# Optimization experiments

Hardware: AMD Instinct MI355X
Metric: run time of the kernel (lower is better)

Reference implementation:

```python
import jax, jax.numpy as jnp
import numpy as np

D_IN = 1024
D_OUT = 1024

def setup_inputs() -> dict:
    key = jax.random.key(0)
    kx, kq, kk, kv = jax.random.split(key, 4)
    X = jax.random.normal(kx, (4, 2048, D_IN), dtype=jnp.float32)
    s = 1.0 / np.sqrt(D_IN)
    Wq = jax.random.uniform(kq, (D_IN, D_OUT), jnp.float32, -s, s)
    Wk = jax.random.uniform(kk, (D_IN, D_OUT), jnp.float32, -s, s)
    Wv = jax.random.uniform(kv, (D_IN, D_OUT), jnp.float32, -s, s)
    return {"X": X, "Wq": Wq, "Wk": Wk, "Wv": Wv}

def reference(X, Wq, Wk, Wv):
    # X: [b, s, d_in]; W*: [d_in, d_out] (torch Linear weight transposed)
    B, S, _ = X.shape
    q = jnp.einsum('bsd,de->bse', X, Wq)
    k = jnp.einsum('bsd,de->bse', X, Wk)
    v = jnp.einsum('bsd,de->bse', X, Wv)
    scores = jnp.einsum('bqe,bke->bqk', q, k)  # [b, s, s]
    causal = jnp.triu(jnp.ones((S, S), dtype=bool), k=1)
    scores = jnp.where(causal, -jnp.inf, scores)
    weights = jax.nn.softmax(scores / jnp.sqrt(jnp.asarray(k.shape[-1], scores.dtype)), axis=-1)
    # dropout p=0.0 (eval) -> identity
    return jnp.einsum('bqk,bke->bqe', weights, v)
```

## Files before the change

### kernel.cpp

```cpp
#include <hip/hip_runtime.h>
#include <cstdint>
#include <cmath>

typedef unsigned short u16;
typedef u16   u16x4  __attribute__((ext_vector_type(4)));
typedef u16   u16x8  __attribute__((ext_vector_type(8)));
typedef __bf16 bf16x8 __attribute__((ext_vector_type(8)));
typedef float f32x4  __attribute__((ext_vector_type(4)));

__device__ __forceinline__ u16 f2bf(float f) {
    uint32_t u = __builtin_bit_cast(uint32_t, f);
    u += 0x7fffu + ((u >> 16) & 1u);
    return (u16)(u >> 16);
}
__device__ __forceinline__ float bf2f(u16 v) {
    uint32_t u = ((uint32_t)v) << 16;
    return __builtin_bit_cast(float, u);
}
__device__ __forceinline__ void gload_lds16(const u16* g, u16* l) {
    __builtin_amdgcn_global_load_lds((const __attribute__((address_space(1))) void*)g,
                                     (__attribute__((address_space(3))) void*)l,
                                     16, 0, 0);
}

__global__ __launch_bounds__(256) void prep_kernel(const float* __restrict__ X,
                                                   const float* __restrict__ Wq,
                                                   const float* __restrict__ Wk,
                                                   const float* __restrict__ Wv,
                                                   u16* __restrict__ Xb,
                                                   u16* __restrict__ Wt) {
    __shared__ u16 tile[64 * 72];
    typedef float f4 __attribute__((ext_vector_type(4)));
    const int bid = blockIdx.x;
    if (bid < 8192) {
        const int idx = bid * 256 + threadIdx.x;
        f4 f = ((const f4*)X)[idx];
        u16x4 o;
        o[0] = f2bf(f[0]); o[1] = f2bf(f[1]); o[2] = f2bf(f[2]); o[3] = f2bf(f[3]);
        ((u16x4*)Xb)[idx] = o;
        return;
    }
    const int id = bid - 8192;
    const int z = id >> 8, rem = id & 255;
    const float* W = (z == 0) ? Wq : (z == 1) ? Wk : Wv;
    u16* out = Wt + ((size_t)z << 20);
    const int nt = (rem & 15) * 64, kt = (rem >> 4) * 64;
    const int t = threadIdx.x, r = t >> 2, cq = (t & 3) * 16;
    const float* src = W + (size_t)(kt + r) * 1024 + nt + cq;
#pragma unroll
    for (int q = 0; q < 4; q++) {
        f4 f = ((const f4*)src)[q];
        tile[r * 72 + cq + q * 4 + 0] = f2bf(f[0]);
        tile[r * 72 + cq + q * 4 + 1] = f2bf(f[1]);
        tile[r * 72 + cq + q * 4 + 2] = f2bf(f[2]);
        tile[r * 72 + cq + q * 4 + 3] = f2bf(f[3]);
    }
    __syncthreads();
    u16x8 o0, o1;
#pragma unroll
    for (int e = 0; e < 8; e++) { o0[e] = tile[(cq + e) * 72 + r]; o1[e] = tile[(cq + 8 + e) * 72 + r]; }
    u16* dst = out + (size_t)(nt + r) * 1024 + kt + cq;
    *(u16x8*)dst = o0;
    *(u16x8*)(dst + 8) = o1;
}

template <int OUTMODE>
__device__ __forceinline__ void gemm_bt_core(u16* __restrict__ smem,
                                             const u16* __restrict__ A,
                                             const u16* __restrict__ Bt,
                                             void* __restrict__ outp,
                                             const int ldk, const int ldo,
                                             const int kbeg, const int kend,
                                             const int m0, const int n0,
                                             const int om0, const int on0) {
    u16* As = smem;
    u16* Bs = smem + 4096;
    const int tid = (int)threadIdx.x;
    const int wave = tid >> 6, lane = tid & 63;
    const int wm = wave >> 1, wn = wave & 1;

    f32x4 acc[4][4] = {};

    const int sr = lane >> 2;
    const int scw = ((lane & 3) ^ ((sr >> 1) & 3)) * 8;
    const u16* gA = A  + (size_t)(m0 + wave * 32 + sr) * ldk + scw;
    const u16* gB = Bt + (size_t)(n0 + wave * 32 + sr) * ldk + scw;
    u16* lA = As + wave * 1024;
    u16* lB = Bs + wave * 1024;
    const size_t rstep = (size_t)ldk * 16;

    const int arow = lane & 15;
    const int ksw  = (arow >> 1) & 3;
    const int koff = (((lane >> 4) ^ ksw)) * 8;
    const u16* pa = As + (wm * 64 + arow) * 32 + koff;
    const u16* pb = Bs + (wn * 64 + arow) * 32 + koff;

    for (int k0 = kbeg; k0 < kend; k0 += 32) {
        gload_lds16(gA + k0,         lA);
        gload_lds16(gA + k0 + rstep, lA + 512);
        gload_lds16(gB + k0,         lB);
        gload_lds16(gB + k0 + rstep, lB + 512);
        __syncthreads();
        bf16x8 a[4], b[4];
#pragma unroll
        for (int i = 0; i < 4; i++) a[i] = *(const bf16x8*)(pa + i * 512);
#pragma unroll
        for (int j = 0; j < 4; j++) b[j] = *(const bf16x8*)(pb + j * 512);
#pragma unroll
        for (int i = 0; i < 4; i++)
#pragma unroll
            for (int j = 0; j < 4; j++)
                acc[i][j] = __builtin_amdgcn_mfma_f32_16x16x32_bf16(a[i], b[j], acc[i][j], 0, 0, 0);
        __syncthreads();
    }

    const int row0 = om0 + wm * 64 + ((lane >> 4) << 2);
    const int col0 = on0 + wn * 64 + (lane & 15);
    if constexpr (OUTMODE == 0) {
        u16* o = (u16*)outp;
#pragma unroll
        for (int i = 0; i < 4; i++)
#pragma unroll
            for (int r = 0; r < 4; r++) {
                u16* po = o + (size_t)(row0 + i * 16 + r) * ldo + col0;
#pragma unroll
                for (int j = 0; j < 4; j++) po[j * 16] = f2bf(acc[i][j][r]);
            }
    } else {
        float* o = (float*)outp;
#pragma unroll
        for (int i = 0; i < 4; i++)
#pragma unroll
            for (int r = 0; r < 4; r++) {
                float* po = o + (size_t)(row0 + i * 16 + r) * ldo + col0;
#pragma unroll
                for (int j = 0; j < 4; j++) po[j * 16] = acc[i][j][r];
            }
    }
}

__global__ __launch_bounds__(512, 2) void qkv_gemm_kernel(const u16* __restrict__ Xb,
                                                          const u16* __restrict__ Wt,
                                                          u16* __restrict__ QKV) {
    __shared__ u16 lds[49152];
    const int bid = blockIdx.x;
    const int xcd = bid & 7, slot = bid >> 3;
    const int z = slot >> 5, r32 = slot & 31;
    const int m0 = (xcd * 4 + (r32 >> 3)) << 8;
    const int n0 = (r32 & 7) << 7;

    const u16* __restrict__ A = Xb;
    const u16* __restrict__ B = Wt + ((size_t)z << 20);
    u16* __restrict__ C = QKV + ((size_t)z << 23);

    const int tid = (int)threadIdx.x;
    const int w = tid >> 6, l = tid & 63;
    const int wm = w >> 2, wn = w & 3;

    const int srow = w * 16 + (l >> 3);
    const int scol = ((l & 7) ^ ((l >> 3) & 7)) * 8;
    const u16* gA = A + (size_t)(m0 + srow) * 1024 + scol;
    const u16* gB = B + (size_t)(n0 + srow) * 1024 + scol;
    u16* const sA = lds + w * 1024;
    u16* const sB = lds + 32768 + w * 1024;

    const int c0 = ((l >> 4) ^ (l & 7)) * 8;
    const u16* const pa_ = lds + (wm * 64 + (l & 15)) * 64;
    const u16* const pb_ = lds + 32768 + (wn * 32 + (l & 15)) * 64;

    f32x4 acc[2][4][2] = {};
    bf16x8 a[4][2], b[2][2];

#define MFMA_ __builtin_amdgcn_mfma_f32_16x16x32_bf16
#define STG_A(BUF, H, T) \
    gload_lds16(gA + (size_t)((H) * 128) * 1024 + (T) * 64,       sA + (BUF) + (H) * 8192); \
    gload_lds16(gA + (size_t)((H) * 128 + 8) * 1024 + (T) * 64,   sA + (BUF) + (H) * 8192 + 512);
#define STG_B(BUF, T) \
    gload_lds16(gB + (T) * 64,                                    sB + ((BUF) >> 1)); \
    gload_lds16(gB + (size_t)8 * 1024 + (T) * 64,                 sB + ((BUF) >> 1) + 512);
#define LD_A(BUF, QA) \
    _Pragma("unroll") for (int m_ = 0; m_ < 4; m_++) { \
        a[m_][0] = *(const bf16x8*)(pa_ + (BUF) + (QA) * 8192 + m_ * 1024 + c0); \
        a[m_][1] = *(const bf16x8*)(pa_ + (BUF) + (QA) * 8192 + m_ * 1024 + (c0 ^ 32)); \
    }
#define LD_B(BUF) \
    _Pragma("unroll") for (int n_ = 0; n_ < 2; n_++) { \
        b[n_][0] = *(const bf16x8*)(pb_ + ((BUF) >> 1) + n_ * 1024 + c0); \
        b[n_][1] = *(const bf16x8*)(pb_ + ((BUF) >> 1) + n_ * 1024 + (c0 ^ 32)); \
    }
#define MM(QA) \
    _Pragma("unroll") for (int m_ = 0; m_ < 4; m_++) { \
        _Pragma("unroll") for (int n_ = 0; n_ < 2; n_++) { \
            acc[QA][m_][n_] = MFMA_(a[m_][0], b[n_][0], acc[QA][m_][n_], 0, 0, 0); \
            acc[QA][m_][n_] = MFMA_(a[m_][1], b[n_][1], acc[QA][m_][n_], 0, 0, 0); \
        } \
    }
#define VM6 asm volatile("s_waitcnt vmcnt(6)" ::: "memory");
#define VM2 asm volatile("s_waitcnt vmcnt(2)" ::: "memory");
#define VM0 asm volatile("s_waitcnt vmcnt(0)" ::: "memory");
#define VMN
#define BAR __builtin_amdgcn_s_barrier();
#define PRIO1 __builtin_amdgcn_s_setprio(1);
#define PRIO0 __builtin_amdgcn_s_setprio(0);
#define TILE(BUF, OBUF, T1, S1, T2, S2, VMA, VMB) \
    LD_A(BUF, 0) LD_B(BUF) \
    if (S1) { STG_A(OBUF, 1, T1) } \
    VMA BAR PRIO1 MM(0) PRIO0 BAR \
    LD_A(BUF, 1) \
    if (S2) { STG_A(BUF, 0, T2) STG_B(BUF, T2) } \
    VMB BAR PRIO1 MM(1) PRIO0 BAR

    STG_A(0, 0, 0) STG_B(0, 0) STG_A(0, 1, 0)
    STG_A(16384, 0, 1) STG_B(16384, 1)
    asm volatile("s_waitcnt vmcnt(6)" ::: "memory");
    __builtin_amdgcn_s_barrier();

#pragma unroll 1
    for (int i = 0; i < 7; ++i) {
        const int t1 = 2 * i + 1, t2 = 2 * i + 2, t3 = 2 * i + 3;
        TILE(0,     16384, t1, 1, t2, 1, VM6, VM6)
        TILE(16384, 0,     t2, 1, t3, 1, VM6, VM6)
    }
    TILE(0,     16384, 15, 1, 0, 0, VM6, VM2)
    TILE(16384, 0,     0,  0, 0, 0, VM0, VMN)

    const int row0 = m0 + wm * 64 + ((l >> 4) << 2);
    const int col0 = n0 + wn * 32 + (l & 15);
#pragma unroll
    for (int qa = 0; qa < 2; qa++)
#pragma unroll
        for (int m = 0; m < 4; m++)
#pragma unroll
            for (int r = 0; r < 4; r++) {
                u16* po = C + (size_t)(row0 + qa * 128 + m * 16 + r) * 1024 + col0;
#pragma unroll
                for (int n = 0; n < 2; n++) po[n * 16] = f2bf(acc[qa][m][n][r]);
            }
#undef MFMA_
#undef STG_A
#undef STG_B
#undef LD_A
#undef LD_B
#undef MM
#undef VM6
#undef VM2
#undef VM0
#undef VMN
#undef BAR
#undef PRIO1
#undef PRIO0
#undef TILE
}

__global__ __launch_bounds__(256) void s_tr_kernel(const u16* __restrict__ QKV,
                                                   u16* __restrict__ S,
                                                   u16* __restrict__ Vt) {
    __shared__ u16 smem[8192];
    const int bid = blockIdx.x;
    if (bid < 576) {
        const int xcd = bid & 7, slot = bid >> 3;
        const int b = xcd >> 1, half = xcd & 1;
        int it = half ? 11 : 0;
        const int ntiles = half ? 70 : 66;
        if (slot >= ntiles) return;
        int acc = 0;
        while (acc + it + 1 <= slot) { acc += it + 1; it++; }
        const int jt = slot - acc;
        const u16* Q  = QKV + ((size_t)b << 21);
        const u16* Kp = QKV + ((size_t)1 << 23) + ((size_t)b << 21);
        gemm_bt_core<0>(smem, Q, Kp, S + ((size_t)b << 22), 1024, 2048, 0, 1024,
                        it * 128, jt * 128, it * 128, jt * 128);
        return;
    }
    const int id = bid - 576;
    const int z = id >> 9, rem = id & 511;
    const u16* src = QKV + ((size_t)2 << 23) + ((size_t)z << 21);
    u16* dst = Vt + ((size_t)z << 21);
    const int st = (rem & 31) * 64, et = (rem >> 5) * 64;
    u16 (*tile)[72] = (u16(*)[72])smem;
    const int t = threadIdx.x, r = t >> 2, cq = (t & 3) * 16;
    const u16* p = src + (size_t)(st + r) * 1024 + et + cq;
    u16x8 u0 = *(const u16x8*)p;
    u16x8 u1 = *(const u16x8*)(p + 8);
#pragma unroll
    for (int e = 0; e < 8; e++) { tile[r][cq + e] = u0[e]; tile[r][cq + 8 + e] = u1[e]; }
    __syncthreads();
    u16x8 o0, o1;
#pragma unroll
    for (int e = 0; e < 8; e++) { o0[e] = tile[cq + e][r]; o1[e] = tile[cq + 8 + e][r]; }
    u16* q = dst + (size_t)(et + r) * 2048 + st + cq;
    *(u16x8*)q = o0;
    *(u16x8*)(q + 8) = o1;
}

__device__ __forceinline__ void pv_tile128(const u16* __restrict__ Pb,
                                           const u16* __restrict__ Vb,
                                           float* __restrict__ Ob,
                                           u16* __restrict__ lds,
                                           const int it, const int n0) {
    const int tid = (int)threadIdx.x;
    const int w = tid >> 6, l = tid & 63;
    const int wm = w >> 2, wn = w & 3;
    const int nk = 2 * (it + 1);
    const int m0 = it * 128;

    const int srow = w * 16 + (l >> 3);
    const int scol = ((l & 7) ^ ((l >> 3) & 7)) * 8;
    const u16* gA = Pb + (size_t)(m0 + srow) * 2048 + scol;
    const u16* gB = Vb + (size_t)(n0 + srow) * 2048 + scol;
    u16* const sA = lds + w * 1024;
    u16* const sB = lds + 24576 + w * 1024;

    const int c0 = ((l >> 4) ^ (l & 7)) * 8;
    const u16* const pa_ = lds + (wm * 64 + (l & 15)) * 64;
    const u16* const pb_ = lds + 24576 + (wn * 32 + (l & 15)) * 64;

    f32x4 acc[4][2] = {};

#define PSTG(T, BUF) \
    gload_lds16(gA + (size_t)(T) * 64,                    sA + (BUF) * 8192); \
    gload_lds16(gA + (size_t)(T) * 64 + (size_t)8 * 2048, sA + (BUF) * 8192 + 512); \
    gload_lds16(gB + (size_t)(T) * 64,                    sB + (BUF) * 8192); \
    gload_lds16(gB + (size_t)(T) * 64 + (size_t)8 * 2048, sB + (BUF) * 8192 + 512);

    PSTG(0, 0) PSTG(1, 1)
    asm volatile("s_waitcnt vmcnt(4)" ::: "memory");
    __builtin_amdgcn_s_barrier();

    int bufR = 0, bufW = 2;
#pragma unroll 1
    for (int t = 0; t < nk; ++t) {
        bf16x8 a[4][2], b[2][2];
#pragma unroll
        for (int m = 0; m < 4; m++) {
            a[m][0] = *(const bf16x8*)(pa_ + bufR * 8192 + m * 1024 + c0);
            a[m][1] = *(const bf16x8*)(pa_ + bufR * 8192 + m * 1024 + (c0 ^ 32));
        }
#pragma unroll
        for (int n = 0; n < 2; n++) {
            b[n][0] = *(const bf16x8*)(pb_ + bufR * 8192 + n * 1024 + c0);
            b[n][1] = *(const bf16x8*)(pb_ + bufR * 8192 + n * 1024 + (c0 ^ 32));
        }
        if (t < nk - 2) {
            PSTG(t + 2, bufW)
            asm volatile("s_waitcnt vmcnt(4)" ::: "memory");
        } else {
            asm volatile("s_waitcnt vmcnt(0)" ::: "memory");
        }
        __builtin_amdgcn_s_barrier();
        __builtin_amdgcn_s_setprio(1);
#pragma unroll
        for (int m = 0; m < 4; m++)
#pragma unroll
            for (int n = 0; n < 2; n++) {
                acc[m][n] = __builtin_amdgcn_mfma_f32_16x16x32_bf16(a[m][0], b[n][0], acc[m][n], 0, 0, 0);
                acc[m][n] = __builtin_amdgcn_mfma_f32_16x16x32_bf16(a[m][1], b[n][1], acc[m][n], 0, 0, 0);
            }
        __builtin_amdgcn_s_setprio(0);
        __builtin_amdgcn_s_barrier();
        bufR = (bufR == 2) ? 0 : bufR + 1;
        bufW = (bufW == 2) ? 0 : bufW + 1;
    }
#undef PSTG

    const int row0 = m0 + wm * 64 + ((l >> 4) << 2);
    const int col0 = n0 + wn * 32 + (l & 15);
#pragma unroll
    for (int m = 0; m < 4; m++)
#pragma unroll
        for (int r = 0; r < 4; r++) {
            float* po = Ob + (size_t)(row0 + m * 16 + r) * 1024 + col0;
#pragma unroll
            for (int n = 0; n < 2; n++) po[n * 16] = acc[m][n][r];
        }
}

__global__ __launch_bounds__(512, 2) void pv_gemm_kernel(const u16* __restrict__ P,
                                                         const u16* __restrict__ Vt,
                                                         float* __restrict__ O) {
    __shared__ u16 lds[49152];
    const int bid = blockIdx.x;
    const int xcd = bid & 7, slot = bid >> 3;
    const int combo = xcd * 4 + (slot >> 3);
    const int n0 = (slot & 7) * 128;
    const int pair = combo >> 2, b = combo & 3;
    const u16* Pb = P + ((size_t)b << 22);
    const u16* Vb = Vt + ((size_t)b << 21);
    float* Ob = O + ((size_t)b << 21);
    pv_tile128(Pb, Vb, Ob, lds, 15 - pair, n0);
    pv_tile128(Pb, Vb, Ob, lds, pair, n0);
}

__global__ __launch_bounds__(256) void softmax_kernel(u16* __restrict__ S) {
    const int wave = threadIdx.x >> 6, lane = threadIdx.x & 63;
    const int g = blockIdx.x * 4 + wave;
    const int b = g >> 11, i = g & 2047;
    u16* row = S + ((size_t)b << 22) + ((size_t)i << 11);
    const int n = i + 1;
    const int kend = ((i >> 7) + 1) << 7;
    const int nt_ = (kend + 511) >> 9;
    const float NEG = -1e30f;
    float v[32];
    float m = NEG;
#pragma unroll
    for (int t = 0; t < 4; t++) {
        if (t < nt_) {
            u16x8 u = *(const u16x8*)(row + t * 512 + lane * 8);
#pragma unroll
            for (int e = 0; e < 8; e++) {
                const int col = t * 512 + lane * 8 + e;
                float f = (col < n) ? bf2f(u[e]) : NEG;
                v[t * 8 + e] = f;
                m = fmaxf(m, f);
            }
        }
    }
#pragma unroll
    for (int off = 32; off > 0; off >>= 1) m = fmaxf(m, __shfl_xor(m, off, 64));
    const float sc = 0.03125f * 1.44269504088896f;
    float s = 0.f;
#pragma unroll
    for (int t = 0; t < 4; t++) {
        if (t < nt_) {
#pragma unroll
            for (int e = 0; e < 8; e++) {
                const float x = v[t * 8 + e];
                const float e2 = (x == NEG) ? 0.f : exp2f((x - m) * sc);
                v[t * 8 + e] = e2;
                s += e2;
            }
        }
    }
#pragma unroll
    for (int off = 32; off > 0; off >>= 1) s += __shfl_xor(s, off, 64);
    const float inv = 1.f / s;
#pragma unroll
    for (int t = 0; t < 4; t++) {
        if (t < nt_) {
            u16x8 o;
#pragma unroll
            for (int e = 0; e < 8; e++) o[e] = f2bf(v[t * 8 + e] * inv);
            *(u16x8*)(row + t * 512 + lane * 8) = o;
        }
    }
}

extern "C" void kernel_launch(void* const* d_in, const int* in_sizes, int n_in,
                              void* d_out, int out_size, void* d_ws, size_t ws_size,
                              hipStream_t stream) {
    const float* X  = (const float*)d_in[0];
    const float* Wq = (const float*)d_in[1];
    const float* Wk = (const float*)d_in[2];
    const float* Wv = (const float*)d_in[3];
    float* out = (float*)d_out;

    u16* ws  = (u16*)d_ws;
    u16* Xb  = ws;
    u16* Wt  = Xb + ((size_t)1 << 23);
    u16* QKV = Wt + 3 * ((size_t)1 << 20);
    u16* S   = QKV + 3 * ((size_t)1 << 23);
    u16* Vt  = Xb;

    prep_kernel<<<8960, 256, 0, stream>>>(X, Wq, Wk, Wv, Xb, Wt);
    qkv_gemm_kernel<<<768, 512, 0, stream>>>(Xb, Wt, QKV);
    s_tr_kernel<<<2624, 256, 0, stream>>>(QKV, S, Vt);
    softmax_kernel<<<2048, 256, 0, stream>>>(S);
    pv_gemm_kernel<<<256, 512, 0, stream>>>(S, Vt, out);
}
```

Before: 219.0 us.

## Fuse Q, K, V projections into one tile sharing the X A-tile

Each workgroup of the QKV GEMM now computes a 128x128 output tile for all three weight matrices at once, instead of a 256x128 tile for a single one. A single X tile is staged in LDS and reused across three B tiles, cutting global reads of X by a factor of three. The grid shrinks from 768 to 512 blocks. LDS grows to 128KB and accumulators grow by 50%, which may reduce occupancy below the declared two blocks per CU and change the pipeline's wait structure.

```diff
diff --git a/kernel.cpp b/kernel.cpp
--- a/kernel.cpp
+++ b/kernel.cpp
@@ -142,16 +142,11 @@
 __global__ __launch_bounds__(512, 2) void qkv_gemm_kernel(const u16* __restrict__ Xb,
                                                           const u16* __restrict__ Wt,
                                                           u16* __restrict__ QKV) {
-    __shared__ u16 lds[49152];
+    __shared__ u16 lds[65536];
     const int bid = blockIdx.x;
     const int xcd = bid & 7, slot = bid >> 3;
-    const int z = slot >> 5, r32 = slot & 31;
-    const int m0 = (xcd * 4 + (r32 >> 3)) << 8;
-    const int n0 = (r32 & 7) << 7;
-
-    const u16* __restrict__ A = Xb;
-    const u16* __restrict__ B = Wt + ((size_t)z << 20);
-    u16* __restrict__ C = QKV + ((size_t)z << 23);
+    const int m0 = (xcd * 8 + (slot >> 3)) << 7;
+    const int n0 = (slot & 7) << 7;
 
     const int tid = (int)threadIdx.x;
     const int w = tid >> 6, l = tid & 63;
@@ -159,83 +154,89 @@
 
     const int srow = w * 16 + (l >> 3);
     const int scol = ((l & 7) ^ ((l >> 3) & 7)) * 8;
-    const u16* gA = A + (size_t)(m0 + srow) * 1024 + scol;
-    const u16* gB = B + (size_t)(n0 + srow) * 1024 + scol;
+    const u16* gA  = Xb + (size_t)(m0 + srow) * 1024 + scol;
+    const u16* gB0 = Wt + (size_t)(n0 + srow) * 1024 + scol;
+    const u16* gB1 = gB0 + ((size_t)1 << 20);
+    const u16* gB2 = gB0 + ((size_t)2 << 20);
     u16* const sA = lds + w * 1024;
-    u16* const sB = lds + 32768 + w * 1024;
+    u16* const sB = lds + 16384 + w * 1024;
 
     const int c0 = ((l >> 4) ^ (l & 7)) * 8;
     const u16* const pa_ = lds + (wm * 64 + (l & 15)) * 64;
-    const u16* const pb_ = lds + 32768 + (wn * 32 + (l & 15)) * 64;
-
-    f32x4 acc[2][4][2] = {};
+    const u16* const pb_ = lds + 16384 + (wn * 32 + (l & 15)) * 64;
+
+    f32x4 acc[3][4][2] = {};
     bf16x8 a[4][2], b[2][2];
 
 #define MFMA_ __builtin_amdgcn_mfma_f32_16x16x32_bf16
-#define STG_A(BUF, H, T) \
-    gload_lds16(gA + (size_t)((H) * 128) * 1024 + (T) * 64,       sA + (BUF) + (H) * 8192); \
-    gload_lds16(gA + (size_t)((H) * 128 + 8) * 1024 + (T) * 64,   sA + (BUF) + (H) * 8192 + 512);
-#define STG_B(BUF, T) \
-    gload_lds16(gB + (T) * 64,                                    sB + ((BUF) >> 1)); \
-    gload_lds16(gB + (size_t)8 * 1024 + (T) * 64,                 sB + ((BUF) >> 1) + 512);
-#define LD_A(BUF, QA) \
+#define STG_A(P, T) \
+    gload_lds16(gA + (size_t)(T) * 64,                    sA + (P) * 8192); \
+    gload_lds16(gA + (size_t)(T) * 64 + (size_t)8 * 1024, sA + (P) * 8192 + 512);
+#define STG_B(P, Z, GB, T) \
+    gload_lds16(GB + (size_t)(T) * 64,                    sB + (Z) * 16384 + (P) * 8192); \
+    gload_lds16(GB + (size_t)(T) * 64 + (size_t)8 * 1024, sB + (Z) * 16384 + (P) * 8192 + 512);
+#define LD_A(P) \
     _Pragma("unroll") for (int m_ = 0; m_ < 4; m_++) { \
-        a[m_][0] = *(const bf16x8*)(pa_ + (BUF) + (QA) * 8192 + m_ * 1024 + c0); \
-        a[m_][1] = *(const bf16x8*)(pa_ + (BUF) + (QA) * 8192 + m_ * 1024 + (c0 ^ 32)); \
-    }
-#define LD_B(BUF) \
+        a[m_][0] = *(const bf16x8*)(pa_ + (P) * 8192 + m_ * 1024 + c0); \
+        a[m_][1] = *(const bf16x8*)(pa_ + (P) * 8192 + m_ * 1024 + (c0 ^ 32)); \
+    }
+#define LD_B(P, Z) \
     _Pragma("unroll") for (int n_ = 0; n_ < 2; n_++) { \
-        b[n_][0] = *(const bf16x8*)(pb_ + ((BUF) >> 1) + n_ * 1024 + c0); \
-        b[n_][1] = *(const bf16x8*)(pb_ + ((BUF) >> 1) + n_ * 1024 + (c0 ^ 32)); \
-    }
-#define MM(QA) \
+        b[n_][0] = *(const bf16x8*)(pb_ + (Z) * 16384 + (P) * 8192 + n_ * 1024 + c0); \
+        b[n_][1] = *(const bf16x8*)(pb_ + (Z) * 16384 + (P) * 8192 + n_ * 1024 + (c0 ^ 32)); \
+    }
+#define MM(Z) \
     _Pragma("unroll") for (int m_ = 0; m_ < 4; m_++) { \
         _Pragma("unroll") for (int n_ = 0; n_ < 2; n_++) { \
-            acc[QA][m_][n_] = MFMA_(a[m_][0], b[n_][0], acc[QA][m_][n_], 0, 0, 0); \
-            acc[QA][m_][n_] = MFMA_(a[m_][1], b[n_][1], acc[QA][m_][n_], 0, 0, 0); \
+            acc[Z][m_][n_] = MFMA_(a[m_][0], b[n_][0], acc[Z][m_][n_], 0, 0, 0); \
+            acc[Z][m_][n_] = MFMA_(a[m_][1], b[n_][1], acc[Z][m_][n_], 0, 0, 0); \
         } \
     }
 #define VM6 asm volatile("s_waitcnt vmcnt(6)" ::: "memory");
-#define VM2 asm volatile("s_waitcnt vmcnt(2)" ::: "memory");
 #define VM0 asm volatile("s_waitcnt vmcnt(0)" ::: "memory");
 #define VMN
 #define BAR __builtin_amdgcn_s_barrier();
 #define PRIO1 __builtin_amdgcn_s_setprio(1);
 #define PRIO0 __builtin_amdgcn_s_setprio(0);
-#define TILE(BUF, OBUF, T1, S1, T2, S2, VMA, VMB) \
-    LD_A(BUF, 0) LD_B(BUF) \
-    if (S1) { STG_A(OBUF, 1, T1) } \
-    VMA BAR PRIO1 MM(0) PRIO0 BAR \
-    LD_A(BUF, 1) \
-    if (S2) { STG_A(BUF, 0, T2) STG_B(BUF, T2) } \
-    VMB BAR PRIO1 MM(1) PRIO0 BAR
-
-    STG_A(0, 0, 0) STG_B(0, 0) STG_A(0, 1, 0)
-    STG_A(16384, 0, 1) STG_B(16384, 1)
+#define TILE(P, S1, T1, S2, T2, VM3) \
+    LD_A(P) LD_B(P, 0) \
+    if (S1) { STG_B((P) ^ 1, 2, gB2, T1) } \
+    BAR PRIO1 MM(0) PRIO0 BAR \
+    LD_B(P, 1) \
+    if (S2) { STG_A(P, T2) STG_B(P, 0, gB0, T2) } \
+    BAR PRIO1 MM(1) PRIO0 BAR \
+    LD_B(P, 2) \
+    if (S2) { STG_B(P, 1, gB1, T2) } \
+    VM3 \
+    BAR PRIO1 MM(2) PRIO0 BAR
+
+    STG_A(0, 0) STG_B(0, 0, gB0, 0) STG_B(0, 1, gB1, 0) STG_B(0, 2, gB2, 0)
+    STG_A(1, 1) STG_B(1, 0, gB0, 1) STG_B(1, 1, gB1, 1)
     asm volatile("s_waitcnt vmcnt(6)" ::: "memory");
     __builtin_amdgcn_s_barrier();
 
 #pragma unroll 1
     for (int i = 0; i < 7; ++i) {
-        const int t1 = 2 * i + 1, t2 = 2 * i + 2, t3 = 2 * i + 3;
-        TILE(0,     16384, t1, 1, t2, 1, VM6, VM6)
-        TILE(16384, 0,     t2, 1, t3, 1, VM6, VM6)
-    }
-    TILE(0,     16384, 15, 1, 0, 0, VM6, VM2)
-    TILE(16384, 0,     0,  0, 0, 0, VM0, VMN)
+        TILE(0, 1, 2 * i + 1, 1, 2 * i + 2, VM6)
+        TILE(1, 1, 2 * i + 2, 1, 2 * i + 3, VM6)
+    }
+    TILE(0, 1, 15, 0, 0, VM0)
+    TILE(1, 0, 0, 0, 0, VMN)
 
     const int row0 = m0 + wm * 64 + ((l >> 4) << 2);
     const int col0 = n0 + wn * 32 + (l & 15);
 #pragma unroll
-    for (int qa = 0; qa < 2; qa++)
+    for (int z = 0; z < 3; z++) {
+        u16* C = QKV + ((size_t)z << 23);
 #pragma unroll
         for (int m = 0; m < 4; m++)
 #pragma unroll
             for (int r = 0; r < 4; r++) {
-                u16* po = C + (size_t)(row0 + qa * 128 + m * 16 + r) * 1024 + col0;
-#pragma unroll
-                for (int n = 0; n < 2; n++) po[n * 16] = f2bf(acc[qa][m][n][r]);
-            }
+                u16* po = C + (size_t)(row0 + m * 16 + r) * 1024 + col0;
+#pragma unroll
+                for (int n = 0; n < 2; n++) po[n * 16] = f2bf(acc[z][m][n][r]);
+            }
+    }
 #undef MFMA_
 #undef STG_A
 #undef STG_B
@@ -243,7 +244,6 @@
 #undef LD_B
 #undef MM
 #undef VM6
-#undef VM2
 #undef VM0
 #undef VMN
 #undef BAR
@@ -462,7 +462,7 @@
     u16* Vt  = Xb;
 
     prep_kernel<<<8960, 256, 0, stream>>>(X, Wq, Wk, Wv, Xb, Wt);
-    qkv_gemm_kernel<<<768, 512, 0, stream>>>(Xb, Wt, QKV);
+    qkv_gemm_kernel<<<512, 512, 0, stream>>>(Xb, Wt, QKV);
     s_tr_kernel<<<2624, 256, 0, stream>>>(QKV, S, Vt);
     softmax_kernel<<<2048, 256, 0, stream>>>(S);
     pv_gemm_kernel<<<256, 512, 0, stream>>>(S, Vt, out);
```

After: 222.5 us. About the same (+1.6%).
